# Kernel tuning notes

Hardware: AMD Instinct MI355X
Metric: run time of the kernel (lower is better)

## Reference

```python
import jax, jax.numpy as jnp
import numpy as np

B, N, LATENT, HIDDEN = 65536, 32, 32, 64

def setup_inputs() -> dict:
    key = jax.random.key(0)
    ks = jax.random.split(key, 16)
    def xavier(k, shape):
        fan_in, fan_out = shape[1], shape[0]
        lim = float(np.sqrt(6.0 / (fan_in + fan_out)))
        return jax.random.uniform(k, shape, jnp.float32, -lim, lim)
    inp = {
        'x_sensors': jax.random.normal(ks[0], (B, N), jnp.float32),
        'state_x': jax.random.uniform(ks[1], (B, 1), jnp.float32),
        # GAT: W Linear(1, LATENT, bias=False), a Linear(2*LATENT, 1, bias=False), xavier init
        'W_gat': xavier(ks[2], (LATENT, 1)),
        'a_gat': xavier(ks[3], (1, 2 * LATENT)),
        # pooling: Linear(LATENT, LATENT//2) -> Tanh -> Linear(LATENT//2, 1) -> Softmax(dim=1)
        'p1_w': xavier(ks[4], (LATENT // 2, LATENT)),
        'p1_b': jnp.zeros((LATENT // 2,), jnp.float32),
        'p2_w': xavier(ks[5], (1, LATENT // 2)),
        'p2_b': jnp.zeros((1,), jnp.float32),
        # MNN: MonotonicLinear raw weights uniform(-0.5, 0.5), zero bias
        'm1_w': jax.random.uniform(ks[6], (HIDDEN, 1), jnp.float32, -0.5, 0.5),
        'm1_b': jnp.zeros((HIDDEN,), jnp.float32),
        'm2_w': jax.random.uniform(ks[7], (HIDDEN, HIDDEN), jnp.float32, -0.5, 0.5),
        'm2_b': jnp.zeros((HIDDEN,), jnp.float32),
        'm3_w': jax.random.uniform(ks[8], (LATENT, HIDDEN), jnp.float32, -0.5, 0.5),
        'm3_b': jnp.zeros((LATENT,), jnp.float32),
    }
    return inp

def reference(x_sensors, state_x, W_gat, a_gat, p1_w, p1_b, p2_w, p2_b,
              m1_w, m1_b, m2_w, m2_b, m3_w, m3_b):
    # --- GAT encoder ---
    # h = x_sensors[..., None] (B,N,1); Wh = h @ W_gat.T -> (B,N,D)
    Wh = jnp.einsum('bn,d->bnd', x_sensors, W_gat[:, 0])
    # e_ij = leakyrelu(a^T [Wh_i || Wh_j]) decomposed: a = [a1; a2]
    a1, a2 = a_gat[0, :LATENT], a_gat[0, LATENT:]
    s_i = jnp.einsum('bnd,d->bn', Wh, a1)  # contribution of Wh_i
    s_j = jnp.einsum('bnd,d->bn', Wh, a2)  # contribution of Wh_j
    e = jax.nn.leaky_relu(s_i[:, :, None] + s_j[:, None, :], 0.2)  # (B,N,N)
    alpha = jax.nn.softmax(e, axis=2)  # dropout is identity in eval
    h_prime = jnp.einsum('bij,bjd->bid', alpha, Wh)  # (B,N,D)
    # pooling: softmax over sensor dim (dim=1)
    t = jnp.tanh(h_prime @ p1_w.T + p1_b)
    beta = jax.nn.softmax(t @ p2_w.T + p2_b, axis=1)  # (B,N,1)
    z_enc = jnp.sum(h_prime * beta, axis=1)  # (B,D)
    # --- MNN decoder (exp-positive weights) ---
    h1 = jnp.tanh(state_x @ jnp.exp(m1_w).T + m1_b)
    h2 = jnp.tanh(h1 @ jnp.exp(m2_w).T + m2_b)
    z_dec = h2 @ jnp.exp(m3_w).T + m3_b  # (B,D)
    return (z_enc, z_dec)
```

## Files before the change

### kernel.cpp

```cpp
#include <hip/hip_runtime.h>
#include <hip/hip_bf16.h>

#define LOG2E     1.4426950408889634f
#define TWO_LOG2E 2.8853900817779268f

typedef __attribute__((ext_vector_type(8))) short    bf16x8;
typedef __attribute__((ext_vector_type(8))) _Float16 f16x8;
typedef __attribute__((ext_vector_type(4))) float    f32x4;
typedef __attribute__((ext_vector_type(2))) float    f32x2;

__device__ __forceinline__ float rcp_(float x){ return __builtin_amdgcn_rcpf(x); }
__device__ __forceinline__ float ex2_(float x){ return __builtin_amdgcn_exp2f(x); }

union FragB { bf16x8 v; uint32_t w[4]; uint4 u4; };
union FragH { f16x8  v; uint32_t w[4]; uint4 u4; };

__device__ __forceinline__ uint16_t f2bf(float x){
  union { __hip_bfloat16 h; uint16_t u; } c; c.h = __float2bfloat16(x); return c.u;
}
__device__ __forceinline__ float bf2f(uint16_t u){
  union { __hip_bfloat16 h; uint16_t u; } c; c.u = u; return __bfloat162float(c.h);
}
__device__ __forceinline__ uint32_t pkh(float a, float b){
  union { _Float16 h; uint16_t u; } ca, cb;
  ca.h = (_Float16)a; cb.h = (_Float16)b;
  return (uint32_t)ca.u | ((uint32_t)cb.u << 16);
}
__device__ __forceinline__ void split2(float a, float b, uint32_t& whi, uint32_t& wlo){
  uint16_t ah = f2bf(a), bh = f2bf(b);
  uint16_t al = f2bf(a - bf2f(ah)), bl_ = f2bf(b - bf2f(bh));
  whi = (uint32_t)ah | ((uint32_t)bh << 16);
  wlo = (uint32_t)al | ((uint32_t)bl_ << 16);
}
__device__ __forceinline__ void expsplit8(const float* __restrict__ src,
                                          FragB& hi, FragB& lo){
  float4 a = *(const float4*)src;
  float4 b = *(const float4*)(src + 4);
  float e0=__expf(a.x), e1=__expf(a.y), e2=__expf(a.z), e3=__expf(a.w);
  float e4=__expf(b.x), e5=__expf(b.y), e6=__expf(b.z), e7=__expf(b.w);
  split2(e0,e1, hi.w[0], lo.w[0]);
  split2(e2,e3, hi.w[1], lo.w[1]);
  split2(e4,e5, hi.w[2], lo.w[2]);
  split2(e6,e7, hi.w[3], lo.w[3]);
}
__device__ __forceinline__ void exph8(const float* __restrict__ src, FragH& out){
  float4 a = *(const float4*)src;
  float4 b = *(const float4*)(src + 4);
  out.w[0] = pkh(__expf(a.x), __expf(a.y));
  out.w[1] = pkh(__expf(a.z), __expf(a.w));
  out.w[2] = pkh(__expf(b.x), __expf(b.y));
  out.w[3] = pkh(__expf(b.z), __expf(b.w));
}

#define TBL_N     512
#define TBL_SCALE 25.6f
#define TBL_LO    -10.0f
#define TBL_CMAX  9.9f

__global__ __launch_bounds__(256, 5) void IDSSM_fused(
    const float* __restrict__ xs,  const float* __restrict__ stx,
    const float* __restrict__ Wg,  const float* __restrict__ ag,
    const float* __restrict__ p1w, const float* __restrict__ p1b,
    const float* __restrict__ p2w, const float* __restrict__ p2b,
    const float* __restrict__ m1w, const float* __restrict__ m1b,
    const float* __restrict__ m2w, const float* __restrict__ m2b,
    const float* __restrict__ m3w, const float* __restrict__ m3b,
    float* __restrict__ out, int B)
{
  __shared__ float xsh[64*33];
  __shared__ uint4 fg1[8][64];
  __shared__ uint4 fg2hi[4][64];
  __shared__ uint4 fg2lo[4][64];
  __shared__ float tbl[TBL_N];
  __shared__ float e1s2[64];
  __shared__ float m1b2s[64];
  __shared__ float qsh[16];
  __shared__ float pbb[16];
  __shared__ float p2wn[16];
  __shared__ float scal[3];

  const int tid = threadIdx.x;
  const int lb  = tid >> 2;
  const int q   = tid & 3;
  const int b0  = blockIdx.x * 64;
  const int b   = b0 + lb;
  const bool valid = (b < B);

  const int lane = tid & 63;
  const int bl_  = lane & 15;
  const int gt_  = lane >> 4;

  {
    int rsrc = b0 + lb; if (rsrc >= B) rsrc = B - 1;
    const float4* src = (const float4*)(xs + (size_t)rsrc*32) + q*2;
    float4 v0 = src[0], v1 = src[1];
    float* dst = xsh + lb*33 + q*8;
    dst[0]=v0.x; dst[1]=v0.y; dst[2]=v0.z; dst[3]=v0.w;
    dst[4]=v1.x; dst[5]=v1.y; dst[6]=v1.z; dst[7]=v1.w;
  }
  #pragma unroll
  for (int rep = 0; rep < 2; ++rep){
    const int s  = (tid >> 6) + 4*rep;
    const int mt = s >> 1, kt = s & 1;
    FragH h;
    exph8(m2w + (bl_ + 16*mt)*64 + 8*gt_ + 32*kt, h);
    fg1[s][lane] = h.u4;
  }
  {
    const int s2  = tid >> 6;
    const int mt2 = s2 >> 1, kt2 = s2 & 1;
    FragB hi, lo;
    expsplit8(m3w + (bl_ + 16*mt2)*64 + 8*gt_ + 32*kt2, hi, lo);
    fg2hi[s2][lane] = hi.u4;
    fg2lo[s2][lane] = lo.u4;
  }
  if (tid < 64){
    e1s2[tid]  = __expf(m1w[tid]) * TWO_LOG2E;
    m1b2s[tid] = m1b[tid] * TWO_LOG2E;
  }
  if (tid >= 64 && tid < 80){
    const int k = tid - 64;
    float acc = 0.f;
    #pragma unroll
    for (int d = 0; d < 32; ++d) acc += p1w[k*32 + d] * Wg[d];
    qsh[k]  = acc * TWO_LOG2E;
    pbb[k]  = p1b[k] * TWO_LOG2E;
    p2wn[k] = -2.f * p2w[k];
  }
  if (tid == 80){
    float A1 = 0.f, A2 = 0.f;
    #pragma unroll
    for (int d = 0; d < 32; ++d){ A1 += Wg[d]*ag[d]; A2 += Wg[d]*ag[32+d]; }
    scal[0] = A1 * LOG2E;
    scal[1] = A2 * LOG2E;
  }
  if (tid == 81){
    float sp = 0.f;
    #pragma unroll
    for (int k = 0; k < 16; ++k) sp += p2w[k];
    scal[2] = sp + p2b[0];
  }
  __syncthreads();

  {
    const float u0 = scal[2];
    #pragma unroll
    for (int rep = 0; rep < 2; ++rep){
      const int n = tid + rep*256;
      const float c = TBL_LO + (float)n * (1.0f/TBL_SCALE);
      float u = u0;
      #pragma unroll
      for (int k = 0; k < 16; ++k){
        float E = ex2_(fmaf(c, qsh[k], pbb[k]));
        u = fmaf(p2wn[k], rcp_(E + 1.f), u);
      }
      tbl[n] = u * LOG2E;
    }
  }
  __syncthreads();

  const float A1p = scal[0], A2p = scal[1];
  const float* xrow = xsh + lb*33;
  f32x2 Ei2[4], Eq2[4], s2[4], sx2[4];
  #pragma unroll
  for (int p = 0; p < 4; ++p){
    float sa = A1p * xrow[q*8 + 2*p];
    float sb = A1p * xrow[q*8 + 2*p + 1];
    Ei2[p] = (f32x2){ ex2_(sa), ex2_(sb) };
    Eq2[p] = (f32x2){ ex2_(0.2f*sa), ex2_(0.2f*sb) };
    s2[p]  = (f32x2)(0.f);
    sx2[p] = (f32x2)(0.f);
  }
  #pragma unroll 4
  for (int j = 0; j < 32; ++j){
    const float xj = xrow[j];
    const float tj = A2p * xj;
    const float Fj = ex2_(tj);
    const float Fq = ex2_(0.2f*tj);
    const f32x2 Fj2 = { Fj, Fj };
    const f32x2 Fq2 = { Fq, Fq };
    const f32x2 xj2 = { xj, xj };
    #pragma unroll
    for (int p = 0; p < 4; ++p){
      f32x2 pa = Ei2[p] * Fj2;
      f32x2 pb = Eq2[p] * Fq2;
      f32x2 pe = __builtin_elementwise_max(pa, pb);
      s2[p]  = s2[p] + pe;
      sx2[p] = sx2[p] + pe * xj2;
    }
  }

  float Zs = 0.f, Zd = 0.f;
  #pragma unroll
  for (int p = 0; p < 4; ++p){
    #pragma unroll
    for (int h = 0; h < 2; ++h){
      const float sv  = h ? s2[p].y  : s2[p].x;
      const float sxv = h ? sx2[p].y : sx2[p].x;
      const float c  = sxv * rcp_(sv);
      const float cc = fminf(fmaxf(c, TBL_LO), TBL_CMAX);
      const float f  = (cc - TBL_LO) * TBL_SCALE;
      const int   n  = (int)f;
      const float fr = f - (float)n;
      const float t0 = tbl[n];
      const float t1 = tbl[n + 1];
      const float u2 = fmaf(fr, t1 - t0, t0);
      const float eb = ex2_(u2);
      Zs = fmaf(eb, c, Zs);
      Zd += eb;
    }
  }
  Zs += __shfl_xor(Zs, 1);  Zd += __shfl_xor(Zd, 1);
  Zs += __shfl_xor(Zs, 2);  Zd += __shfl_xor(Zd, 2);
  const float Z = Zs * rcp_(Zd);

  if (valid){
    const float4 w0 = ((const float4*)Wg)[q*2 + 0];
    const float4 w1 = ((const float4*)Wg)[q*2 + 1];
    float4* o = (float4*)(out + (size_t)b*32 + q*8);
    o[0] = make_float4(Z*w0.x, Z*w0.y, Z*w0.z, Z*w0.w);
    o[1] = make_float4(Z*w1.x, Z*w1.y, Z*w1.z, Z*w1.w);
  }

  const int wv = tid >> 6;
  const int gt = gt_;
  const int bl = bl_;
  const int bd = b0 + wv*16 + bl;
  const float sx0 = stx[(bd < B) ? bd : (B-1)];

  FragH h1f[2];
  #pragma unroll
  for (int kt = 0; kt < 2; ++kt){
    const int g0 = 8*gt + 32*kt;
    float hv[8];
    #pragma unroll
    for (int j = 0; j < 8; ++j){
      float E = ex2_(fmaf(sx0, e1s2[g0+j], m1b2s[g0+j]));
      hv[j] = fmaf(-2.f, rcp_(E + 1.f), 1.f);
    }
    #pragma unroll
    for (int jw = 0; jw < 4; ++jw)
      h1f[kt].w[jw] = pkh(hv[2*jw], hv[2*jw+1]);
  }

  f32x4 acc[4];
  #pragma unroll
  for (int mt = 0; mt < 4; ++mt){
    float4 bi = *(const float4*)(m2b + 16*mt + 4*gt);
    acc[mt][0]=bi.x; acc[mt][1]=bi.y; acc[mt][2]=bi.z; acc[mt][3]=bi.w;
  }
  #pragma unroll
  for (int mt = 0; mt < 4; ++mt){
    #pragma unroll
    for (int kt = 0; kt < 2; ++kt){
      FragH A; A.u4 = fg1[mt*2+kt][lane];
      acc[mt] = __builtin_amdgcn_mfma_f32_16x16x32_f16(A.v, h1f[kt].v, acc[mt], 0, 0, 0);
    }
  }

  uint32_t Whi[4][2], Wlo[4][2];
  #pragma unroll
  for (int mt = 0; mt < 4; ++mt){
    float t0 = fmaf(-2.f, rcp_(ex2_(acc[mt][0]*TWO_LOG2E) + 1.f), 1.f);
    float t1 = fmaf(-2.f, rcp_(ex2_(acc[mt][1]*TWO_LOG2E) + 1.f), 1.f);
    float t2 = fmaf(-2.f, rcp_(ex2_(acc[mt][2]*TWO_LOG2E) + 1.f), 1.f);
    float t3 = fmaf(-2.f, rcp_(ex2_(acc[mt][3]*TWO_LOG2E) + 1.f), 1.f);
    split2(t0, t1, Whi[mt][0], Wlo[mt][0]);
    split2(t2, t3, Whi[mt][1], Wlo[mt][1]);
  }

  FragB B2hi[2], B2lo[2];
  const int hiSel = gt >> 1;
  #pragma unroll
  for (int kt2 = 0; kt2 < 2; ++kt2){
    #pragma unroll
    for (int jw = 0; jw < 4; ++jw){
      const int sl = bl + 16*(((jw>>1) + 2*gt) & 3);
      const int w  = jw & 1;
      uint32_t c0 = (uint32_t)__shfl((int)Whi[2*kt2+0][w], sl);
      uint32_t c1 = (uint32_t)__shfl((int)Whi[2*kt2+1][w], sl);
      B2hi[kt2].w[jw] = hiSel ? c1 : c0;
      uint32_t d0 = (uint32_t)__shfl((int)Wlo[2*kt2+0][w], sl);
      uint32_t d1 = (uint32_t)__shfl((int)Wlo[2*kt2+1][w], sl);
      B2lo[kt2].w[jw] = hiSel ? d1 : d0;
    }
  }

  f32x4 acc2[2];
  #pragma unroll
  for (int mt2 = 0; mt2 < 2; ++mt2){
    float4 bi = *(const float4*)(m3b + 16*mt2 + 4*gt);
    acc2[mt2][0]=bi.x; acc2[mt2][1]=bi.y; acc2[mt2][2]=bi.z; acc2[mt2][3]=bi.w;
  }
  #pragma unroll
  for (int mt2 = 0; mt2 < 2; ++mt2){
    #pragma unroll
    for (int kt2 = 0; kt2 < 2; ++kt2){
      FragB Ahi, Alo;
      Ahi.u4 = fg2hi[mt2*2 + kt2][lane];
      Alo.u4 = fg2lo[mt2*2 + kt2][lane];
      acc2[mt2] = __builtin_amdgcn_mfma_f32_16x16x32_bf16(Ahi.v, B2hi[kt2].v, acc2[mt2], 0, 0, 0);
      acc2[mt2] = __builtin_amdgcn_mfma_f32_16x16x32_bf16(Ahi.v, B2lo[kt2].v, acc2[mt2], 0, 0, 0);
      acc2[mt2] = __builtin_amdgcn_mfma_f32_16x16x32_bf16(Alo.v, B2hi[kt2].v, acc2[mt2], 0, 0, 0);
    }
  }

  if (bd < B){
    float* o = out + (size_t)B*32 + (size_t)bd*32;
    *(float4*)(o + 4*gt)      = make_float4(acc2[0][0], acc2[0][1], acc2[0][2], acc2[0][3]);
    *(float4*)(o + 16 + 4*gt) = make_float4(acc2[1][0], acc2[1][1], acc2[1][2], acc2[1][3]);
  }
}

extern "C" void kernel_launch(void* const* d_in, const int* in_sizes, int n_in,
                              void* d_out, int out_size, void* d_ws, size_t ws_size,
                              hipStream_t stream)
{
  const float* xs  = (const float*)d_in[0];
  const float* stx = (const float*)d_in[1];
  const float* Wg  = (const float*)d_in[2];
  const float* ag  = (const float*)d_in[3];
  const float* p1w = (const float*)d_in[4];
  const float* p1b = (const float*)d_in[5];
  const float* p2w = (const float*)d_in[6];
  const float* p2b = (const float*)d_in[7];
  const float* m1w = (const float*)d_in[8];
  const float* m1b = (const float*)d_in[9];
  const float* m2w = (const float*)d_in[10];
  const float* m2b = (const float*)d_in[11];
  const float* m3w = (const float*)d_in[12];
  const float* m3b = (const float*)d_in[13];
  float* out = (float*)d_out;
  const int B = in_sizes[0] / 32;
  const int nblk = (B + 63) / 64;
  hipLaunchKernelGGL(IDSSM_fused, dim3(nblk), dim3(256), 0, stream,
                     xs, stx, Wg, ag, p1w, p1b, p2w, p2b,
                     m1w, m1b, m2w, m2b, m3w, m3b, out, B);
}
```

Before: 26.52 us.

## Split weight preprocessing into a prologue kernel and read fragments from workspace

Weight-dependent precomputation (exp of MNN weights into MFMA fragments, the pooling lookup table, attention scalars) moves out of every block into a small 5-block prologue kernel that writes to the workspace. The main kernel loads these from global memory, keeps fragments in registers instead of LDS, and drops the LDS staging of x rows. The per-row attention loop now broadcasts exp factors across the quad with DPP instead of recomputing exp per j. This removes redundant per-block exp/table work and most LDS use, at the cost of a second launch, more registers, and global reads of the workspace.

```diff
diff --git a/kernel.cpp b/kernel.cpp
--- a/kernel.cpp
+++ b/kernel.cpp
@@ -11,6 +11,12 @@
 
 __device__ __forceinline__ float rcp_(float x){ return __builtin_amdgcn_rcpf(x); }
 __device__ __forceinline__ float ex2_(float x){ return __builtin_amdgcn_exp2f(x); }
+
+template<int K>
+__device__ __forceinline__ float quadbc(float v){
+  constexpr int ctrl = K * 0x55;
+  return __int_as_float(__builtin_amdgcn_mov_dpp(__float_as_int(v), ctrl, 0xf, 0xf, true));
+}
 
 union FragB { bf16x8 v; uint32_t w[4]; uint4 u4; };
 union FragH { f16x8  v; uint32_t w[4]; uint4 u4; };
@@ -52,143 +58,152 @@
   out.w[3] = pkh(__expf(b.z), __expf(b.w));
 }
 
+#define WS_FG1   0
+#define WS_FG2H  2048
+#define WS_FG2L  3072
+#define WS_TBL   4096
+#define WS_E1S   4608
+#define WS_M1B   4672
+#define WS_SCAL  4736
+
 #define TBL_N     512
 #define TBL_SCALE 25.6f
 #define TBL_LO    -10.0f
 #define TBL_CMAX  9.9f
 
-__global__ __launch_bounds__(256, 5) void IDSSM_fused(
-    const float* __restrict__ xs,  const float* __restrict__ stx,
+__global__ __launch_bounds__(256) void IDSSM_pre(
     const float* __restrict__ Wg,  const float* __restrict__ ag,
     const float* __restrict__ p1w, const float* __restrict__ p1b,
     const float* __restrict__ p2w, const float* __restrict__ p2b,
     const float* __restrict__ m1w, const float* __restrict__ m1b,
-    const float* __restrict__ m2w, const float* __restrict__ m2b,
-    const float* __restrict__ m3w, const float* __restrict__ m3b,
+    const float* __restrict__ m2w, const float* __restrict__ m3w,
+    float* __restrict__ ws)
+{
+  const int blk = blockIdx.x;
+  const int tid = threadIdx.x;
+  const int l  = tid & 63;
+  const int bl = l & 15, gt = l >> 4;
+  if (blk < 2){
+    const int s  = (blk*256 + tid) >> 6;
+    const int mt = s >> 1, kt = s & 1;
+    FragH h;
+    exph8(m2w + (bl + 16*mt)*64 + 8*gt + 32*kt, h);
+    *(uint4*)(ws + WS_FG1 + (size_t)(s*64 + l)*4) = h.u4;
+  } else if (blk == 2){
+    const int s2  = tid >> 6;
+    const int mt2 = s2 >> 1, kt2 = s2 & 1;
+    FragB hi, lo;
+    expsplit8(m3w + (bl + 16*mt2)*64 + 8*gt + 32*kt2, hi, lo);
+    *(uint4*)(ws + WS_FG2H + (size_t)(s2*64 + l)*4) = hi.u4;
+    *(uint4*)(ws + WS_FG2L + (size_t)(s2*64 + l)*4) = lo.u4;
+  } else if (blk == 3){
+    __shared__ float qs[16], pb_[16], pw[16], u0s[1];
+    if (tid < 16){
+      float acc = 0.f;
+      #pragma unroll
+      for (int d = 0; d < 32; ++d) acc += p1w[tid*32 + d] * Wg[d];
+      qs[tid]  = acc * TWO_LOG2E;
+      pb_[tid] = p1b[tid] * TWO_LOG2E;
+      pw[tid]  = -2.f * p2w[tid];
+    }
+    if (tid == 16){
+      float sp = 0.f;
+      #pragma unroll
+      for (int k = 0; k < 16; ++k) sp += p2w[k];
+      u0s[0] = sp + p2b[0];
+    }
+    __syncthreads();
+    #pragma unroll
+    for (int rep = 0; rep < 2; ++rep){
+      const int n = tid + rep*256;
+      const float c = TBL_LO + (float)n * (1.0f/TBL_SCALE);
+      float u = u0s[0];
+      #pragma unroll
+      for (int k = 0; k < 16; ++k){
+        float E = ex2_(fmaf(c, qs[k], pb_[k]));
+        u = fmaf(pw[k], rcp_(E + 1.f), u);
+      }
+      ws[WS_TBL + n] = u * LOG2E;
+    }
+  } else {
+    if (tid < 64){
+      ws[WS_E1S + tid] = __expf(m1w[tid]) * TWO_LOG2E;
+      ws[WS_M1B + tid] = m1b[tid] * TWO_LOG2E;
+    } else if (tid == 64){
+      float A1 = 0.f, A2 = 0.f;
+      #pragma unroll
+      for (int d = 0; d < 32; ++d){ A1 += Wg[d]*ag[d]; A2 += Wg[d]*ag[32+d]; }
+      ws[WS_SCAL + 0] = A1 * LOG2E;
+      ws[WS_SCAL + 1] = A2 * LOG2E;
+    }
+  }
+}
+
+#define XJ(J) (((((J)&3))==0) ? xr4[(J)>>2].x : ((((J)&3))==1) ? xr4[(J)>>2].y : \
+               ((((J)&3))==2) ? xr4[(J)>>2].z : xr4[(J)>>2].w)
+
+#define ATT_J(JQ, JR) { \
+    const float Fj_ = quadbc<JQ>(Fjr[JR]); \
+    const float Fq_ = quadbc<JQ>(Fqr[JR]); \
+    const float xj_ = XJ(JQ*8+JR); \
+    const f32x2 Fj2_ = {Fj_,Fj_}, Fq2_ = {Fq_,Fq_}, xj2_ = {xj_,xj_}; \
+    f32x2 pe_; \
+    pe_ = __builtin_elementwise_max(Ei2[0]*Fj2_, Eq2[0]*Fq2_); s2[0] = s2[0] + pe_; sx2[0] = sx2[0] + pe_*xj2_; \
+    pe_ = __builtin_elementwise_max(Ei2[1]*Fj2_, Eq2[1]*Fq2_); s2[1] = s2[1] + pe_; sx2[1] = sx2[1] + pe_*xj2_; \
+    pe_ = __builtin_elementwise_max(Ei2[2]*Fj2_, Eq2[2]*Fq2_); s2[2] = s2[2] + pe_; sx2[2] = sx2[2] + pe_*xj2_; \
+    pe_ = __builtin_elementwise_max(Ei2[3]*Fj2_, Eq2[3]*Fq2_); s2[3] = s2[3] + pe_; sx2[3] = sx2[3] + pe_*xj2_; \
+  }
+#define ATT_Q(JQ) ATT_J(JQ,0) ATT_J(JQ,1) ATT_J(JQ,2) ATT_J(JQ,3) \
+                  ATT_J(JQ,4) ATT_J(JQ,5) ATT_J(JQ,6) ATT_J(JQ,7)
+
+__global__ __launch_bounds__(256, 4) void IDSSM_main(
+    const float* __restrict__ xs,  const float* __restrict__ stx,
+    const float* __restrict__ Wg,  const float* __restrict__ m2b,
+    const float* __restrict__ m3b, const float* __restrict__ ws,
     float* __restrict__ out, int B)
 {
-  __shared__ float xsh[64*33];
-  __shared__ uint4 fg1[8][64];
-  __shared__ uint4 fg2hi[4][64];
-  __shared__ uint4 fg2lo[4][64];
   __shared__ float tbl[TBL_N];
-  __shared__ float e1s2[64];
-  __shared__ float m1b2s[64];
-  __shared__ float qsh[16];
-  __shared__ float pbb[16];
-  __shared__ float p2wn[16];
-  __shared__ float scal[3];
-
   const int tid = threadIdx.x;
   const int lb  = tid >> 2;
   const int q   = tid & 3;
   const int b0  = blockIdx.x * 64;
   const int b   = b0 + lb;
   const bool valid = (b < B);
-
-  const int lane = tid & 63;
-  const int bl_  = lane & 15;
-  const int gt_  = lane >> 4;
-
-  {
-    int rsrc = b0 + lb; if (rsrc >= B) rsrc = B - 1;
-    const float4* src = (const float4*)(xs + (size_t)rsrc*32) + q*2;
-    float4 v0 = src[0], v1 = src[1];
-    float* dst = xsh + lb*33 + q*8;
-    dst[0]=v0.x; dst[1]=v0.y; dst[2]=v0.z; dst[3]=v0.w;
-    dst[4]=v1.x; dst[5]=v1.y; dst[6]=v1.z; dst[7]=v1.w;
-  }
-  #pragma unroll
-  for (int rep = 0; rep < 2; ++rep){
-    const int s  = (tid >> 6) + 4*rep;
-    const int mt = s >> 1, kt = s & 1;
-    FragH h;
-    exph8(m2w + (bl_ + 16*mt)*64 + 8*gt_ + 32*kt, h);
-    fg1[s][lane] = h.u4;
-  }
-  {
-    const int s2  = tid >> 6;
-    const int mt2 = s2 >> 1, kt2 = s2 & 1;
-    FragB hi, lo;
-    expsplit8(m3w + (bl_ + 16*mt2)*64 + 8*gt_ + 32*kt2, hi, lo);
-    fg2hi[s2][lane] = hi.u4;
-    fg2lo[s2][lane] = lo.u4;
-  }
-  if (tid < 64){
-    e1s2[tid]  = __expf(m1w[tid]) * TWO_LOG2E;
-    m1b2s[tid] = m1b[tid] * TWO_LOG2E;
-  }
-  if (tid >= 64 && tid < 80){
-    const int k = tid - 64;
-    float acc = 0.f;
-    #pragma unroll
-    for (int d = 0; d < 32; ++d) acc += p1w[k*32 + d] * Wg[d];
-    qsh[k]  = acc * TWO_LOG2E;
-    pbb[k]  = p1b[k] * TWO_LOG2E;
-    p2wn[k] = -2.f * p2w[k];
-  }
-  if (tid == 80){
-    float A1 = 0.f, A2 = 0.f;
-    #pragma unroll
-    for (int d = 0; d < 32; ++d){ A1 += Wg[d]*ag[d]; A2 += Wg[d]*ag[32+d]; }
-    scal[0] = A1 * LOG2E;
-    scal[1] = A2 * LOG2E;
-  }
-  if (tid == 81){
-    float sp = 0.f;
-    #pragma unroll
-    for (int k = 0; k < 16; ++k) sp += p2w[k];
-    scal[2] = sp + p2b[0];
-  }
-  __syncthreads();
-
-  {
-    const float u0 = scal[2];
-    #pragma unroll
-    for (int rep = 0; rep < 2; ++rep){
-      const int n = tid + rep*256;
-      const float c = TBL_LO + (float)n * (1.0f/TBL_SCALE);
-      float u = u0;
-      #pragma unroll
-      for (int k = 0; k < 16; ++k){
-        float E = ex2_(fmaf(c, qsh[k], pbb[k]));
-        u = fmaf(p2wn[k], rcp_(E + 1.f), u);
-      }
-      tbl[n] = u * LOG2E;
-    }
-  }
-  __syncthreads();
-
-  const float A1p = scal[0], A2p = scal[1];
-  const float* xrow = xsh + lb*33;
+  const int rsrc = valid ? b : (B - 1);
+
+  const float2 tco = *(const float2*)(ws + WS_TBL + tid*2);
+  const float A1p = ws[WS_SCAL + 0];
+  const float A2p = ws[WS_SCAL + 1];
+
+  const float4* xrow4 = (const float4*)(xs + (size_t)rsrc*32);
+  float4 xr4[8];
+  #pragma unroll
+  for (int t = 0; t < 8; ++t) xr4[t] = xrow4[t];
+  float4 xia = xrow4[q*2], xib = xrow4[q*2 + 1];
+  float xi[8] = { xia.x, xia.y, xia.z, xia.w, xib.x, xib.y, xib.z, xib.w };
+
+  tbl[tid*2]     = tco.x;
+  tbl[tid*2 + 1] = tco.y;
+
+  float Fjr[8], Fqr[8];
+  #pragma unroll
+  for (int t = 0; t < 8; ++t){
+    const float tv = A2p * xi[t];
+    Fjr[t] = ex2_(tv);
+    Fqr[t] = ex2_(0.2f * tv);
+  }
   f32x2 Ei2[4], Eq2[4], s2[4], sx2[4];
   #pragma unroll
   for (int p = 0; p < 4; ++p){
-    float sa = A1p * xrow[q*8 + 2*p];
-    float sb = A1p * xrow[q*8 + 2*p + 1];
+    const float sa = A1p * xi[2*p], sb = A1p * xi[2*p + 1];
     Ei2[p] = (f32x2){ ex2_(sa), ex2_(sb) };
     Eq2[p] = (f32x2){ ex2_(0.2f*sa), ex2_(0.2f*sb) };
     s2[p]  = (f32x2)(0.f);
     sx2[p] = (f32x2)(0.f);
   }
-  #pragma unroll 4
-  for (int j = 0; j < 32; ++j){
-    const float xj = xrow[j];
-    const float tj = A2p * xj;
-    const float Fj = ex2_(tj);
-    const float Fq = ex2_(0.2f*tj);
-    const f32x2 Fj2 = { Fj, Fj };
-    const f32x2 Fq2 = { Fq, Fq };
-    const f32x2 xj2 = { xj, xj };
-    #pragma unroll
-    for (int p = 0; p < 4; ++p){
-      f32x2 pa = Ei2[p] * Fj2;
-      f32x2 pb = Eq2[p] * Fq2;
-      f32x2 pe = __builtin_elementwise_max(pa, pb);
-      s2[p]  = s2[p] + pe;
-      sx2[p] = sx2[p] + pe * xj2;
-    }
-  }
+  ATT_Q(0) ATT_Q(1) ATT_Q(2) ATT_Q(3)
+
+  __syncthreads();
 
   float Zs = 0.f, Zd = 0.f;
   #pragma unroll
@@ -204,8 +219,7 @@
       const float fr = f - (float)n;
       const float t0 = tbl[n];
       const float t1 = tbl[n + 1];
-      const float u2 = fmaf(fr, t1 - t0, t0);
-      const float eb = ex2_(u2);
+      const float eb = ex2_(fmaf(fr, t1 - t0, t0));
       Zs = fmaf(eb, c, Zs);
       Zd += eb;
     }
@@ -222,20 +236,32 @@
     o[1] = make_float4(Z*w1.x, Z*w1.y, Z*w1.z, Z*w1.w);
   }
 
-  const int wv = tid >> 6;
-  const int gt = gt_;
-  const int bl = bl_;
-  const int bd = b0 + wv*16 + bl;
+  const int lane = tid & 63;
+  const int wv   = tid >> 6;
+  const int gt   = lane >> 4;
+  const int bl   = lane & 15;
+  const int bd   = b0 + wv*16 + bl;
   const float sx0 = stx[(bd < B) ? bd : (B-1)];
+
+  uint4 fg1r[8];
+  #pragma unroll
+  for (int s = 0; s < 8; ++s)
+    fg1r[s] = *(const uint4*)(ws + WS_FG1 + (size_t)(s*64 + lane)*4);
 
   FragH h1f[2];
   #pragma unroll
   for (int kt = 0; kt < 2; ++kt){
     const int g0 = 8*gt + 32*kt;
+    const float4* e1p = (const float4*)(ws + WS_E1S + g0);
+    const float4* m1p = (const float4*)(ws + WS_M1B + g0);
+    float4 ea = e1p[0], eb4 = e1p[1];
+    float4 ma = m1p[0], mb4 = m1p[1];
+    float ev[8] = { ea.x,ea.y,ea.z,ea.w, eb4.x,eb4.y,eb4.z,eb4.w };
+    float mv[8] = { ma.x,ma.y,ma.z,ma.w, mb4.x,mb4.y,mb4.z,mb4.w };
     float hv[8];
     #pragma unroll
     for (int j = 0; j < 8; ++j){
-      float E = ex2_(fmaf(sx0, e1s2[g0+j], m1b2s[g0+j]));
+      float E = ex2_(fmaf(sx0, ev[j], mv[j]));
       hv[j] = fmaf(-2.f, rcp_(E + 1.f), 1.f);
     }
     #pragma unroll
@@ -253,9 +279,16 @@
   for (int mt = 0; mt < 4; ++mt){
     #pragma unroll
     for (int kt = 0; kt < 2; ++kt){
-      FragH A; A.u4 = fg1[mt*2+kt][lane];
+      FragH A; A.u4 = fg1r[mt*2 + kt];
       acc[mt] = __builtin_amdgcn_mfma_f32_16x16x32_f16(A.v, h1f[kt].v, acc[mt], 0, 0, 0);
     }
+  }
+
+  uint4 fg2h[4], fg2l[4];
+  #pragma unroll
+  for (int s = 0; s < 4; ++s){
+    fg2h[s] = *(const uint4*)(ws + WS_FG2H + (size_t)(s*64 + lane)*4);
+    fg2l[s] = *(const uint4*)(ws + WS_FG2L + (size_t)(s*64 + lane)*4);
   }
 
   uint32_t Whi[4][2], Wlo[4][2];
@@ -297,8 +330,8 @@
     #pragma unroll
     for (int kt2 = 0; kt2 < 2; ++kt2){
       FragB Ahi, Alo;
-      Ahi.u4 = fg2hi[mt2*2 + kt2][lane];
-      Alo.u4 = fg2lo[mt2*2 + kt2][lane];
+      Ahi.u4 = fg2h[mt2*2 + kt2];
+      Alo.u4 = fg2l[mt2*2 + kt2];
       acc2[mt2] = __builtin_amdgcn_mfma_f32_16x16x32_bf16(Ahi.v, B2hi[kt2].v, acc2[mt2], 0, 0, 0);
       acc2[mt2] = __builtin_amdgcn_mfma_f32_16x16x32_bf16(Ahi.v, B2lo[kt2].v, acc2[mt2], 0, 0, 0);
       acc2[mt2] = __builtin_amdgcn_mfma_f32_16x16x32_bf16(Alo.v, B2hi[kt2].v, acc2[mt2], 0, 0, 0);
@@ -331,9 +364,12 @@
   const float* m3w = (const float*)d_in[12];
   const float* m3b = (const float*)d_in[13];
   float* out = (float*)d_out;
+  float* ws  = (float*)d_ws;
   const int B = in_sizes[0] / 32;
+
+  hipLaunchKernelGGL(IDSSM_pre, dim3(5), dim3(256), 0, stream,
+                     Wg, ag, p1w, p1b, p2w, p2b, m1w, m1b, m2w, m3w, ws);
   const int nblk = (B + 63) / 64;
-  hipLaunchKernelGGL(IDSSM_fused, dim3(nblk), dim3(256), 0, stream,
-                     xs, stx, Wg, ag, p1w, p1b, p2w, p2b,
-                     m1w, m1b, m2w, m2b, m3w, m3b, out, B);
-}
+  hipLaunchKernelGGL(IDSSM_main, dim3(nblk), dim3(256), 0, stream,
+                     xs, stx, Wg, m2b, m3b, ws, out, B);
+}
```

New measurement: 25.74 us. 2.9% less time.
